# Kernel tuning notes

Measured on AMD Instinct MI355X. Metric: run time of the kernel, lower is better.

## Reference

```python
import jax, jax.numpy as jnp
import numpy as np

SIZE = (128, 128, 256)  # (H, W, F) SOM grid + feature dim


def setup_inputs() -> dict:
    key = jax.random.key(0)
    k1, k2 = jax.random.split(key)
    xb = jax.random.normal(k1, (4096, SIZE[2]), dtype=jnp.float32)
    weights = jax.random.normal(k2, SIZE, dtype=jnp.float32)
    return {"xb": xb, "weights": weights}


def reference(xb, weights):
    """SOM forward: pairwise Euclidean distances xb vs flattened codebook,
    then argmin -> 2-D BMU grid coordinates. Returns bmus [B, 2] int32."""
    H, W, F = SIZE
    w = weights.reshape(H * W, F)                       # [M, F]
    x_sq = jnp.sum(xb * xb, axis=-1, keepdims=True)     # [B, 1]
    w_sq = jnp.sum(w * w, axis=-1)                      # [M]
    d2 = x_sq - 2.0 * (xb @ w.T) + w_sq                 # [B, M]
    min_idx = jnp.argmin(d2, axis=-1)                   # sqrt is monotone -> same argmin
    bmus = jnp.stack([min_idx // W, min_idx % W], axis=1)
    return bmus
```

## Files before the change

kernel.cpp:

```cpp
#include <hip/hip_runtime.h>


#define B_ROWS 4096
#define M_COLS 16384
#define KF 256
#define BM 128
#define NCHUNK 16
#define NSTEP 32
#define MARGIN 0.75f

typedef _Float16 f16x8 __attribute__((ext_vector_type(8)));
typedef float f32x4 __attribute__((ext_vector_type(4)));
typedef unsigned long long u64;

#define GLOAD16(gsrc, ldst) \
  __builtin_amdgcn_global_load_lds((const __attribute__((address_space(1))) void*)(gsrc), \
                                   (__attribute__((address_space(3))) void*)(ldst), 16, 0, 0)

__device__ __forceinline__ size_t tm_idx(int tile, int ks, int kch, int r) {
    return ((((size_t)(tile * 8 + ks)) * 4 + kch) * 128 + r) * 8;
}

__device__ __forceinline__ unsigned fkey(float s) {
    const unsigned u = __float_as_uint(s);
    return u ^ ((unsigned)((int)u >> 31) | 0x80000000u);
}
__device__ __forceinline__ float unkey(unsigned k) {
    return (k & 0x80000000u) ? __uint_as_float(k & 0x7fffffffu) : __uint_as_float(~k);
}

__global__ __launch_bounds__(256) void som_split(const float* __restrict__ xb,
                                                 const float* __restrict__ wt,
                                                 _Float16* __restrict__ xh,
                                                 _Float16* __restrict__ wh,
                                                 float* __restrict__ wsq) {
    const int bid = blockIdx.x;
    const bool isx = bid < (B_ROWS * 32) / 256;
    const int gid = (isx ? bid : bid - (B_ROWS * 32) / 256) * 256 + threadIdx.x;
    const float* src = isx ? xb : wt;
    _Float16* dst = isx ? xh : wh;
    const int row = gid >> 5;
    const int kg = gid & 31;
    const float4 v0 = *reinterpret_cast<const float4*>(src + (size_t)row * KF + kg * 8);
    const float4 v1 = *reinterpret_cast<const float4*>(src + (size_t)row * KF + kg * 8 + 4);
    const float vv[8] = {v0.x, v0.y, v0.z, v0.w, v1.x, v1.y, v1.z, v1.w};
    f16x8 h;
    float s = 0.0f;
#pragma unroll
    for (int j = 0; j < 8; ++j) {
        h[j] = (_Float16)vv[j];
        s += vv[j] * vv[j];
    }
    *reinterpret_cast<f16x8*>(dst + tm_idx(row >> 7, kg >> 2, kg & 3, row & 127)) = h;
    if (!isx) {
#pragma unroll
        for (int off = 16; off > 0; off >>= 1) s += __shfl_down(s, off, 64);
        if (kg == 0) wsq[row] = s;
    }
}

__global__ __launch_bounds__(256, 2) void som_main(const _Float16* __restrict__ xh,
                                                   const _Float16* __restrict__ wh,
                                                   const float* __restrict__ wsq,
                                                   u64* __restrict__ plist) {
    __shared__ _Float16 lds[2][2][8192];

    const int tid = threadIdx.x;
    const int lane = tid & 63;
    const int frow = lane & 15;
    const int kch = lane >> 4;
    const int wid = tid >> 6;
    const int wr = wid >> 1;
    const int wc = wid & 1;

    const int id = blockIdx.x;
    const int swz = (id & 7) * 64 + (id >> 3);
    const int bx = swz & 31;
    const int by = swz >> 5;
    const int rowbase = bx * BM;

    const int ebase = (tid & 192) * 8;
    const int tid8 = tid * 8;

    float b1v[16], b2v[16];
    unsigned b1c[16];
#pragma unroll
    for (int i = 0; i < 16; ++i) { b1v[i] = b2v[i] = 3.4e38f; b1c[i] = 0u; }

    f32x4 acc[4][4];

#define STAGE(buf_, step_) do {                                               \
    const int ct_ = (step_) >> 2, t_ = (step_) & 3;                           \
    const size_t ab_ = (size_t)(bx * 8 + 2 * t_) * 4096;                      \
    const size_t bb_ = (size_t)((by * 8 + ct_) * 8 + 2 * t_) * 4096;          \
    GLOAD16(xh + ab_ + tid8,        &lds[buf_][0][ebase]);                    \
    GLOAD16(xh + ab_ + 2048 + tid8, &lds[buf_][0][2048 + ebase]);             \
    GLOAD16(xh + ab_ + 4096 + tid8, &lds[buf_][0][4096 + ebase]);             \
    GLOAD16(xh + ab_ + 6144 + tid8, &lds[buf_][0][6144 + ebase]);             \
    GLOAD16(wh + bb_ + tid8,        &lds[buf_][1][ebase]);                    \
    GLOAD16(wh + bb_ + 2048 + tid8, &lds[buf_][1][2048 + ebase]);             \
    GLOAD16(wh + bb_ + 4096 + tid8, &lds[buf_][1][4096 + ebase]);             \
    GLOAD16(wh + bb_ + 6144 + tid8, &lds[buf_][1][6144 + ebase]);             \
  } while (0)

    STAGE(0, 0);
    int buf = 0;

    for (int step = 0; step < NSTEP; ++step) {
        __syncthreads();
        if (step < NSTEP - 1) STAGE(buf ^ 1, step + 1);

        if ((step & 3) == 0) {
#pragma unroll
            for (int m = 0; m < 4; ++m)
#pragma unroll
                for (int n = 0; n < 4; ++n) acc[m][n] = (f32x4){0.f, 0.f, 0.f, 0.f};
        }

#pragma unroll
        for (int kk = 0; kk < 2; ++kk) {
            f16x8 bh[4];
#pragma unroll
            for (int n = 0; n < 4; ++n)
                bh[n] = *reinterpret_cast<const f16x8*>(
                    &lds[buf][1][kk * 4096 + kch * 1024 + (wc * 64 + n * 16 + frow) * 8]);
#pragma unroll
            for (int m = 0; m < 4; ++m) {
                const f16x8 ah = *reinterpret_cast<const f16x8*>(
                    &lds[buf][0][kk * 4096 + kch * 1024 + (wr * 64 + m * 16 + frow) * 8]);
#pragma unroll
                for (int n = 0; n < 4; ++n)
                    acc[m][n] = __builtin_amdgcn_mfma_f32_16x16x32_f16(ah, bh[n], acc[m][n], 0, 0, 0);
            }
        }

        if ((step & 3) == 3) {
            const int ct = step >> 2;
            const int cb = by * 1024 + ct * 128 + wc * 64 + frow;
            float wq[4];
#pragma unroll
            for (int n = 0; n < 4; ++n) wq[n] = wsq[cb + n * 16];
#pragma unroll
            for (int i = 0; i < 16; ++i) {
                const int m = i >> 2, r = i & 3;
                const float s0 = fmaf(-2.0f, acc[m][0][r], wq[0]);
                const float s1 = fmaf(-2.0f, acc[m][1][r], wq[1]);
                const float s2 = fmaf(-2.0f, acc[m][2][r], wq[2]);
                const float s3 = fmaf(-2.0f, acc[m][3][r], wq[3]);
                const float lo01 = fminf(s0, s1), hi01 = fmaxf(s0, s1);
                const float lo23 = fminf(s2, s3), hi23 = fmaxf(s2, s3);
                const unsigned c01 = s0 <= s1 ? (unsigned)cb : (unsigned)(cb + 16);
                const unsigned c23 = s2 <= s3 ? (unsigned)(cb + 32) : (unsigned)(cb + 48);
                const float l1 = fminf(lo01, lo23);
                const unsigned cl = lo01 <= lo23 ? c01 : c23;
                const float l2 = fminf(fminf(hi01, hi23), fmaxf(lo01, lo23));
                const bool q = l1 < b1v[i];
                const float disp = q ? b1v[i] : l1;
                b1c[i] = q ? cl : b1c[i];
                b1v[i] = fminf(l1, b1v[i]);
                b2v[i] = fminf(fminf(disp, l2), b2v[i]);
            }
        }
        buf ^= 1;
    }
#undef STAGE

#pragma unroll
    for (int i = 0; i < 16; ++i) {
        const int rowg = rowbase + wr * 64 + (i >> 2) * 16 + kch * 4 + (i & 3);
        const u64 e = ((u64)fkey(b1v[i]) << 32) |
                      ((u64)(fkey(b2v[i]) >> 14) << 14) | (u64)(b1c[i] & 0x3FFFu);
        plist[(size_t)rowg * 512 + by * 32 + frow * 2 + wc] = e;
    }
}

__global__ __launch_bounds__(256) void som_rescore(const float* __restrict__ xb,
                                                   const float* __restrict__ wt,
                                                   const float* __restrict__ wsq,
                                                   const u64* __restrict__ plist,
                                                   int* __restrict__ out) {
    const int row = (blockIdx.x * 256 + threadIdx.x) >> 6;
    const int lane = threadIdx.x & 63;
    if (row >= B_ROWS) return;
    const float4 xv = *reinterpret_cast<const float4*>(xb + (size_t)row * KF + lane * 4);

    u64 ev[8];
    unsigned g = 0xFFFFFFFFu;
#pragma unroll
    for (int sw = 0; sw < 8; ++sw) {
        ev[sw] = plist[(size_t)row * 512 + sw * 64 + lane];
        const unsigned b1 = (unsigned)(ev[sw] >> 32);
        g = b1 < g ? b1 : g;
    }
#pragma unroll
    for (int mkx = 1; mkx <= 32; mkx <<= 1) {
        const unsigned o = __shfl_xor(g, mkx, 64);
        g = o < g ? o : g;
    }
    const unsigned thr_key = fkey(unkey(g) + MARGIN);
    const unsigned thr_t = thr_key >> 14;

    u64 best = ~0ull;
#pragma unroll
    for (int sw = 0; sw < 8; ++sw) {
        const unsigned b1 = (unsigned)(ev[sw] >> 32);
        const unsigned b2t = (unsigned)(ev[sw] >> 14) & 0x3FFFFu;
        const bool scan = b2t <= thr_t;
        unsigned long long mask = __ballot(b1 <= thr_key && !scan);
        while (mask) {
            const int s0 = __ffsll(mask) - 1; mask &= mask - 1;
            const bool two = mask != 0ull;
            int s1 = s0;
            if (two) { s1 = __ffsll(mask) - 1; mask &= mask - 1; }
            const int col0 = (int)(__shfl(ev[sw], s0, 64) & 0x3FFFull);
            const int col1 = (int)(__shfl(ev[sw], s1, 64) & 0x3FFFull);
            const float4 w0 = *reinterpret_cast<const float4*>(wt + (size_t)col0 * KF + lane * 4);
            float d0 = xv.x * w0.x + xv.y * w0.y + xv.z * w0.z + xv.w * w0.w;
            float d1 = 0.0f;
            if (two) {
                const float4 w1 = *reinterpret_cast<const float4*>(wt + (size_t)col1 * KF + lane * 4);
                d1 = xv.x * w1.x + xv.y * w1.y + xv.z * w1.z + xv.w * w1.w;
            }
#pragma unroll
            for (int mkx = 1; mkx <= 32; mkx <<= 1) {
                d0 += __shfl_xor(d0, mkx, 64);
                d1 += __shfl_xor(d1, mkx, 64);
            }
            const u64 q0 = ((u64)fkey(wsq[col0] - 2.0f * d0) << 32) | (unsigned)col0;
            if (q0 < best) best = q0;
            if (two) {
                const u64 q1 = ((u64)fkey(wsq[col1] - 2.0f * d1) << 32) | (unsigned)col1;
                if (q1 < best) best = q1;
            }
        }
        unsigned long long mask2 = __ballot(scan);
        while (mask2) {
            const int src = __ffsll(mask2) - 1;
            mask2 &= mask2 - 1;
            const int s = sw * 64 + src;
            const int chunk = s >> 5, frs = (s & 31) >> 1, wcs = s & 1;
#pragma unroll
            for (int ct = 0; ct < 8; ++ct) {
                float d[4];
                int colv[4];
#pragma unroll
                for (int n = 0; n < 4; ++n) {
                    colv[n] = chunk * 1024 + ct * 128 + wcs * 64 + n * 16 + frs;
                    const float4 wv = *reinterpret_cast<const float4*>(wt + (size_t)colv[n] * KF + lane * 4);
                    d[n] = xv.x * wv.x + xv.y * wv.y + xv.z * wv.z + xv.w * wv.w;
                }
#pragma unroll
                for (int mkx = 1; mkx <= 32; mkx <<= 1)
#pragma unroll
                    for (int n = 0; n < 4; ++n) d[n] += __shfl_xor(d[n], mkx, 64);
#pragma unroll
                for (int n = 0; n < 4; ++n) {
                    const u64 q = ((u64)fkey(wsq[colv[n]] - 2.0f * d[n]) << 32) | (unsigned)colv[n];
                    if (q < best) best = q;
                }
            }
        }
    }

    if (lane == 0) {
        const int idx = (int)(best & 0xffffffffu);
        out[2 * row] = idx >> 7;
        out[2 * row + 1] = idx & 127;
    }
}

extern "C" void kernel_launch(void* const* d_in, const int* in_sizes, int n_in,
                              void* d_out, int out_size, void* d_ws, size_t ws_size,
                              hipStream_t stream) {
    const float* xb = (const float*)d_in[0];
    const float* wt = (const float*)d_in[1];
    int* out = (int*)d_out;

    char* ws = (char*)d_ws;
    _Float16* xh  = (_Float16*)(ws);
    _Float16* wh  = (_Float16*)(ws + (size_t)2 * 1024 * 1024);
    float*    wsq = (float*)(ws + (size_t)10 * 1024 * 1024);
    u64*    plist = (u64*)(ws + (size_t)11 * 1024 * 1024);

    som_split<<<(B_ROWS * 32 + M_COLS * 32) / 256, 256, 0, stream>>>(xb, wt, xh, wh, wsq);
    som_main<<<BM * NCHUNK / 4, 256, 0, stream>>>(xh, wh, wsq, plist);
    som_rescore<<<B_ROWS / 4, 256, 0, stream>>>(xb, wt, wsq, plist, out);
}
```

Before: 63.31 us.

## Halve per-step K staging and double column chunks to raise occupancy

Each main-kernel step now stages one K-slice (32) instead of two, so LDS per block halves and launch bounds ask for 4 blocks per CU. The codebook is split into 32 chunks of 512 columns, which doubles the grid. To keep the plist layout at 512 entries per row, per-lane top-2 results are merged across lane pairs (xor 8) before being written. The rescore kernel's candidate expansion is updated to the new chunk mapping. The trade-off is more syncs per K, smaller per-block reuse, and more A-tile reloads, in exchange for better latency hiding.

New measurement: 72.73 us. 1.15x slower.

```diff
diff --git a/kernel.cpp b/kernel.cpp
--- a/kernel.cpp
+++ b/kernel.cpp
@@ -5,7 +5,7 @@
 #define M_COLS 16384
 #define KF 256
 #define BM 128
-#define NCHUNK 16
+#define NCHUNK 32
 #define NSTEP 32
 #define MARGIN 0.75f
 
@@ -59,11 +59,11 @@
     }
 }
 
-__global__ __launch_bounds__(256, 2) void som_main(const _Float16* __restrict__ xh,
+__global__ __launch_bounds__(256, 4) void som_main(const _Float16* __restrict__ xh,
                                                    const _Float16* __restrict__ wh,
                                                    const float* __restrict__ wsq,
                                                    u64* __restrict__ plist) {
-    __shared__ _Float16 lds[2][2][8192];
+    __shared__ _Float16 lds[2][2][4096];
 
     const int tid = threadIdx.x;
     const int lane = tid & 63;
@@ -74,7 +74,7 @@
     const int wc = wid & 1;
 
     const int id = blockIdx.x;
-    const int swz = (id & 7) * 64 + (id >> 3);
+    const int swz = (id & 7) * 128 + (id >> 3);
     const int bx = swz & 31;
     const int by = swz >> 5;
     const int rowbase = bx * BM;
@@ -90,17 +90,13 @@
     f32x4 acc[4][4];
 
 #define STAGE(buf_, step_) do {                                               \
-    const int ct_ = (step_) >> 2, t_ = (step_) & 3;                           \
-    const size_t ab_ = (size_t)(bx * 8 + 2 * t_) * 4096;                      \
-    const size_t bb_ = (size_t)((by * 8 + ct_) * 8 + 2 * t_) * 4096;          \
+    const int ct_ = (step_) >> 3, ks_ = (step_) & 7;                          \
+    const size_t ab_ = (size_t)(bx * 8 + ks_) * 4096;                         \
+    const size_t bb_ = (size_t)((by * 4 + ct_) * 8 + ks_) * 4096;             \
     GLOAD16(xh + ab_ + tid8,        &lds[buf_][0][ebase]);                    \
     GLOAD16(xh + ab_ + 2048 + tid8, &lds[buf_][0][2048 + ebase]);             \
-    GLOAD16(xh + ab_ + 4096 + tid8, &lds[buf_][0][4096 + ebase]);             \
-    GLOAD16(xh + ab_ + 6144 + tid8, &lds[buf_][0][6144 + ebase]);             \
     GLOAD16(wh + bb_ + tid8,        &lds[buf_][1][ebase]);                    \
     GLOAD16(wh + bb_ + 2048 + tid8, &lds[buf_][1][2048 + ebase]);             \
-    GLOAD16(wh + bb_ + 4096 + tid8, &lds[buf_][1][4096 + ebase]);             \
-    GLOAD16(wh + bb_ + 6144 + tid8, &lds[buf_][1][6144 + ebase]);             \
   } while (0)
 
     STAGE(0, 0);
@@ -110,33 +106,30 @@
         __syncthreads();
         if (step < NSTEP - 1) STAGE(buf ^ 1, step + 1);
 
-        if ((step & 3) == 0) {
+        if ((step & 7) == 0) {
 #pragma unroll
             for (int m = 0; m < 4; ++m)
 #pragma unroll
                 for (int n = 0; n < 4; ++n) acc[m][n] = (f32x4){0.f, 0.f, 0.f, 0.f};
         }
 
-#pragma unroll
-        for (int kk = 0; kk < 2; ++kk) {
-            f16x8 bh[4];
+        f16x8 bh[4];
+#pragma unroll
+        for (int n = 0; n < 4; ++n)
+            bh[n] = *reinterpret_cast<const f16x8*>(
+                &lds[buf][1][kch * 1024 + (wc * 64 + n * 16 + frow) * 8]);
+#pragma unroll
+        for (int m = 0; m < 4; ++m) {
+            const f16x8 ah = *reinterpret_cast<const f16x8*>(
+                &lds[buf][0][kch * 1024 + (wr * 64 + m * 16 + frow) * 8]);
 #pragma unroll
             for (int n = 0; n < 4; ++n)
-                bh[n] = *reinterpret_cast<const f16x8*>(
-                    &lds[buf][1][kk * 4096 + kch * 1024 + (wc * 64 + n * 16 + frow) * 8]);
-#pragma unroll
-            for (int m = 0; m < 4; ++m) {
-                const f16x8 ah = *reinterpret_cast<const f16x8*>(
-                    &lds[buf][0][kk * 4096 + kch * 1024 + (wr * 64 + m * 16 + frow) * 8]);
-#pragma unroll
-                for (int n = 0; n < 4; ++n)
-                    acc[m][n] = __builtin_amdgcn_mfma_f32_16x16x32_f16(ah, bh[n], acc[m][n], 0, 0, 0);
-            }
-        }
-
-        if ((step & 3) == 3) {
-            const int ct = step >> 2;
-            const int cb = by * 1024 + ct * 128 + wc * 64 + frow;
+                acc[m][n] = __builtin_amdgcn_mfma_f32_16x16x32_f16(ah, bh[n], acc[m][n], 0, 0, 0);
+        }
+
+        if ((step & 7) == 7) {
+            const int ct = step >> 3;
+            const int cb = by * 512 + ct * 128 + wc * 64 + frow;
             float wq[4];
 #pragma unroll
             for (int n = 0; n < 4; ++n) wq[n] = wsq[cb + n * 16];
@@ -167,10 +160,18 @@
 
 #pragma unroll
     for (int i = 0; i < 16; ++i) {
-        const int rowg = rowbase + wr * 64 + (i >> 2) * 16 + kch * 4 + (i & 3);
-        const u64 e = ((u64)fkey(b1v[i]) << 32) |
-                      ((u64)(fkey(b2v[i]) >> 14) << 14) | (u64)(b1c[i] & 0x3FFFu);
-        plist[(size_t)rowg * 512 + by * 32 + frow * 2 + wc] = e;
+        const float o1v = __shfl_xor(b1v[i], 8, 64);
+        const unsigned o1c = __shfl_xor(b1c[i], 8, 64);
+        const float o2v = __shfl_xor(b2v[i], 8, 64);
+        const float n1 = fminf(b1v[i], o1v);
+        const unsigned n1c = b1v[i] <= o1v ? b1c[i] : o1c;
+        const float n2 = fminf(fmaxf(b1v[i], o1v), fminf(b2v[i], o2v));
+        if ((lane & 8) == 0) {
+            const int rowg = rowbase + wr * 64 + (i >> 2) * 16 + kch * 4 + (i & 3);
+            const u64 e = ((u64)fkey(n1) << 32) |
+                          ((u64)(fkey(n2) >> 14) << 14) | (u64)(n1c & 0x3FFFu);
+            plist[(size_t)rowg * 512 + by * 16 + (frow & 7) * 2 + wc] = e;
+        }
     }
 }
 
@@ -238,27 +239,29 @@
             const int src = __ffsll(mask2) - 1;
             mask2 &= mask2 - 1;
             const int s = sw * 64 + src;
-            const int chunk = s >> 5, frs = (s & 31) >> 1, wcs = s & 1;
-#pragma unroll
-            for (int ct = 0; ct < 8; ++ct) {
-                float d[4];
-                int colv[4];
-#pragma unroll
-                for (int n = 0; n < 4; ++n) {
-                    colv[n] = chunk * 1024 + ct * 128 + wcs * 64 + n * 16 + frs;
-                    const float4 wv = *reinterpret_cast<const float4*>(wt + (size_t)colv[n] * KF + lane * 4);
-                    d[n] = xv.x * wv.x + xv.y * wv.y + xv.z * wv.z + xv.w * wv.w;
+            const int chunk = s >> 4, fr8 = (s & 15) >> 1, wcs = s & 1;
+#pragma unroll
+            for (int ct = 0; ct < 4; ++ct)
+#pragma unroll
+                for (int h = 0; h < 2; ++h) {
+                    float d[4];
+                    int colv[4];
+#pragma unroll
+                    for (int n = 0; n < 4; ++n) {
+                        colv[n] = chunk * 512 + ct * 128 + wcs * 64 + n * 16 + fr8 + h * 8;
+                        const float4 wv = *reinterpret_cast<const float4*>(wt + (size_t)colv[n] * KF + lane * 4);
+                        d[n] = xv.x * wv.x + xv.y * wv.y + xv.z * wv.z + xv.w * wv.w;
+                    }
+#pragma unroll
+                    for (int mkx = 1; mkx <= 32; mkx <<= 1)
+#pragma unroll
+                        for (int n = 0; n < 4; ++n) d[n] += __shfl_xor(d[n], mkx, 64);
+#pragma unroll
+                    for (int n = 0; n < 4; ++n) {
+                        const u64 q = ((u64)fkey(wsq[colv[n]] - 2.0f * d[n]) << 32) | (unsigned)colv[n];
+                        if (q < best) best = q;
+                    }
                 }
-#pragma unroll
-                for (int mkx = 1; mkx <= 32; mkx <<= 1)
-#pragma unroll
-                    for (int n = 0; n < 4; ++n) d[n] += __shfl_xor(d[n], mkx, 64);
-#pragma unroll
-                for (int n = 0; n < 4; ++n) {
-                    const u64 q = ((u64)fkey(wsq[colv[n]] - 2.0f * d[n]) << 32) | (unsigned)colv[n];
-                    if (q < best) best = q;
-                }
-            }
         }
     }
 
```
